# Kernel optimization log

Measured on AMD Instinct MI355X. Metric: run time of the kernel, lower is better.

Reference implementation:

```python
import jax, jax.numpy as jnp
import numpy as np

B, LF, RATE = 2, 2048, 4
DF, DS, H = 1024, 1024, 8
D2 = DF // 2            # 512: both self (d1) and cross (d2) branch dims (equal split)
POOL_H = 2048
TS = LF // RATE         # 512 slow steps


def _p(key, shape):
    return jax.random.normal(key, shape, jnp.float32) * 0.02


def setup_inputs() -> dict:
    keys = iter(jax.random.split(jax.random.key(0), 32))
    inp = {
        "x_fast": jax.random.normal(next(keys), (B, LF, DF), jnp.float32),
        "x_slow": jax.random.normal(next(keys), (B, TS, DS), jnp.float32),
    }
    for name in ("fself", "fcross", "sself", "scross"):
        inp[f"{name}_wqkv"] = _p(next(keys), (D2, 3 * D2))
        inp[f"{name}_bqkv"] = jnp.zeros((3 * D2,), jnp.float32)
        inp[f"{name}_wo"] = _p(next(keys), (D2, D2))
        inp[f"{name}_bo"] = jnp.zeros((D2,), jnp.float32)
    inp["lift_w"] = _p(next(keys), (DS, D2))
    inp["lift_b"] = jnp.zeros((D2,), jnp.float32)
    inp["pool_w1"] = _p(next(keys), (RATE * DF, POOL_H))
    inp["pool_b1"] = jnp.zeros((POOL_H,), jnp.float32)
    inp["pool_w2"] = _p(next(keys), (POOL_H, D2))
    inp["pool_b2"] = jnp.zeros((D2,), jnp.float32)
    return inp


def _mha(q_in, k_in, v_in, wqkv, bqkv, wo, bo):
    """Standard multihead attention with fused in-proj weight [d, 3d]."""
    b, tq, d = q_in.shape
    hd = d // H
    q = q_in @ wqkv[:, :d] + bqkv[:d]
    k = k_in @ wqkv[:, d:2 * d] + bqkv[d:2 * d]
    v = v_in @ wqkv[:, 2 * d:] + bqkv[2 * d:]
    q = q.reshape(b, tq, H, hd)
    k = k.reshape(b, k_in.shape[1], H, hd)
    v = v.reshape(b, v_in.shape[1], H, hd)
    scores = jnp.einsum('bqhd,bkhd->bhqk', q, k) * np.float32(1.0 / np.sqrt(hd))
    w = jax.nn.softmax(scores, axis=-1)
    o = jnp.einsum('bhqk,bkhd->bqhd', w, v).reshape(b, tq, d)
    return o @ wo + bo


def _forward(x_fast, x_slow,
             fself_wqkv, fself_bqkv, fself_wo, fself_bo,
             fcross_wqkv, fcross_bqkv, fcross_wo, fcross_bo,
             sself_wqkv, sself_bqkv, sself_wo, sself_bo,
             scross_wqkv, scross_bqkv, scross_wo, scross_bo,
             lift_w, lift_b, pool_w1, pool_b1, pool_w2, pool_b2):
    b = x_fast.shape[0]
    # ---- fast level: lift slow -> fast timescale (ffn applied before repeat)
    y = jnp.repeat(x_slow @ lift_w + lift_b, RATE, axis=1)          # [B, LF, D2]
    x1, x2 = x_fast[..., :D2], x_fast[..., D2:]
    z_fast = jnp.concatenate([
        _mha(x1, x1, x1, fself_wqkv, fself_bqkv, fself_wo, fself_bo),
        _mha(x2, y, y, fcross_wqkv, fcross_bqkv, fcross_wo, fcross_bo),
    ], axis=-1)
    # ---- slow level: causal block pooling of fast sequence
    blocks = x_fast.reshape(b, TS, RATE * DF)                        # LF == TS*RATE
    s = jax.nn.gelu(blocks @ pool_w1 + pool_b1) @ pool_w2 + pool_b2  # [B, TS, D2]
    # causal shift: prepend zero slow step, drop last (zero in pooled feature dim)
    s = jnp.concatenate([jnp.zeros((b, 1, D2), s.dtype), s[:, :-1]], axis=1)
    s1, s2 = x_slow[..., :D2], x_slow[..., D2:]
    z_slow = jnp.concatenate([
        _mha(s1, s1, s1, sself_wqkv, sself_bqkv, sself_wo, sself_bo),
        _mha(s2, s, s, scross_wqkv, scross_bqkv, scross_wo, scross_bo),
    ], axis=-1)
    return z_fast, z_slow


def reference(x_fast, x_slow,
              fself_wqkv, fself_bqkv, fself_wo, fself_bo,
              fcross_wqkv, fcross_bqkv, fcross_wo, fcross_bo,
              sself_wqkv, sself_bqkv, sself_wo, sself_bo,
              scross_wqkv, scross_bqkv, scross_wo, scross_bo,
              lift_w, lift_b, pool_w1, pool_b1, pool_w2, pool_b2):
    return _forward(x_fast, x_slow,
                    fself_wqkv, fself_bqkv, fself_wo, fself_bo,
                    fcross_wqkv, fcross_bqkv, fcross_wo, fcross_bo,
                    sself_wqkv, sself_bqkv, sself_wo, sself_bo,
                    scross_wqkv, scross_bqkv, scross_wo, scross_bo,
                    lift_w, lift_b, pool_w1, pool_b1, pool_w2, pool_b2)
```

## Files before the change

### kernel.cpp

```cpp
#include <hip/hip_runtime.h>
#include <hip/hip_bf16.h>


typedef __attribute__((ext_vector_type(8))) short bf16x8;
typedef __attribute__((ext_vector_type(4))) float f32x4;
typedef unsigned short u16;
typedef unsigned int u32;

__device__ inline u16 f2bf(float f) {
    __hip_bfloat16 h = __float2bfloat16(f);
    return *reinterpret_cast<u16*>(&h);
}
__device__ inline u32 pack2(float a, float b) {
    return (u32)f2bf(a) | ((u32)f2bf(b) << 16);
}
__device__ inline float bf2f(u16 h) {
    u32 x = ((u32)h) << 16; float f;
    __builtin_memcpy(&f, &x, 4);
    return f;
}
__device__ inline void gld16(const u16* g, u16* l) {
    __builtin_amdgcn_global_load_lds(
        (const __attribute__((address_space(1))) void*)(g),
        (__attribute__((address_space(3))) void*)(l), 16, 0, 0);
}

struct GDesc {
    const u16* A; const u16* Bt; const float* bias;
    void* out0; u16* aux0; u16* aux1;
    int lda, ldb, ldc, K, ntx, mode, rshift, tile_end;
};
struct GPack { int n; int pad[3]; GDesc d[8]; };

template <int TMT>
__global__ __launch_bounds__(256)
void gemm_multi(GPack pk)
{
    constexpr int TM = TMT * 16;
    constexpr int W = TMT / 2;
    __shared__ u16 As[TM * 64];
    __shared__ u16 Bs[TM * 64];

    int bid = blockIdx.x;
    int di = 0;
    while (bid >= pk.d[di].tile_end) ++di;
    const GDesc g = pk.d[di];
    const int base = di ? pk.d[di - 1].tile_end : 0;
    const int local = bid - base;
    const int ty = local / g.ntx, tx = local - ty * g.ntx;
    const int row0 = ty * TM, col0 = tx * TM;

    const int t = threadIdx.x;
    const int wave = t >> 6, lane = t & 63;
    const int l15 = lane & 15, quad = lane >> 4;
    const int wm = (wave >> 1) * W * 16, wn = (wave & 1) * W * 16;

    const int srow = wave * 8 + (lane >> 3);
    const int ssw = (((lane & 7) ^ (lane >> 3))) * 8;
    const u16* Ag = g.A + (long long)(row0 + srow) * g.lda + ssw;
    const u16* Bg = g.Bt + (long long)(col0 + srow) * g.ldb + ssw;

    const int c0 = (quad ^ (l15 & 7)) * 8;

    f32x4 acc[W][W];
#pragma unroll
    for (int i = 0; i < W; ++i)
#pragma unroll
        for (int j = 0; j < W; ++j) {
            acc[i][j][0] = 0.f; acc[i][j][1] = 0.f;
            acc[i][j][2] = 0.f; acc[i][j][3] = 0.f;
        }

    for (int k0 = 0; k0 < g.K; k0 += 64) {
        __syncthreads();
#pragma unroll
        for (int r = 0; r < TM / 32; ++r) {
            gld16(Ag + (long long)r * 32 * g.lda + k0, As + r * 2048 + wave * 512);
            gld16(Bg + (long long)r * 32 * g.ldb + k0, Bs + r * 2048 + wave * 512);
        }
        __syncthreads();
#pragma unroll
        for (int kc = 0; kc < 2; ++kc) {
            const int cc = kc ? (c0 ^ 32) : c0;
            bf16x8 af[W], bfr[W];
#pragma unroll
            for (int i = 0; i < W; ++i) {
                af[i]  = *(const bf16x8*)(As + (wm + i * 16 + l15) * 64 + cc);
                bfr[i] = *(const bf16x8*)(Bs + (wn + i * 16 + l15) * 64 + cc);
            }
#pragma unroll
            for (int i = 0; i < W; ++i)
#pragma unroll
                for (int j = 0; j < W; ++j)
                    acc[i][j] = __builtin_amdgcn_mfma_f32_16x16x32_bf16(af[i], bfr[j], acc[i][j], 0, 0, 0);
        }
    }

    const int rmask = (1 << g.rshift) - 1;
#pragma unroll
    for (int i = 0; i < W; ++i)
#pragma unroll
        for (int j = 0; j < W; ++j)
#pragma unroll
            for (int r = 0; r < 4; ++r) {
                int m = row0 + wm + i * 16 + quad * 4 + r;
                int n = col0 + wn + j * 16 + l15;
                float v = acc[i][j][r];
                if (g.mode != 5) v += g.bias[n];
                if (g.mode == 0) {
                    ((float*)g.out0)[(long long)m * g.ldc + n] = v;
                } else if (g.mode == 1 || g.mode == 5) {
                    ((u16*)g.out0)[(long long)m * g.ldc + n] = f2bf(v);
                } else if (g.mode == 2) {
                    float x3 = v * v * v;
                    v = 0.5f * v * (1.f + tanhf(0.7978845608028654f * (v + 0.044715f * x3)));
                    ((u16*)g.out0)[(long long)m * g.ldc + n] = f2bf(v);
                } else if (g.mode == 3) {
                    u16 h = f2bf(v);
                    if (n < 512) ((u16*)g.out0)[(long long)m * 512 + n] = h;
                    else if (n < 1024) g.aux0[(long long)m * 512 + (n - 512)] = h;
                    else {
                        int d = n - 1024;
                        int bb = m >> g.rshift, rr = m & rmask;
                        g.aux1[((long long)((bb * 8 + (d >> 6)) * 64 + (d & 63)) << g.rshift) + rr] = h;
                    }
                } else if (g.mode == 4) {
                    u16 h = f2bf(v);
                    if (n < 512) ((u16*)g.out0)[(long long)m * 512 + n] = h;
                    else {
                        int d = n - 512;
                        int bb = m >> g.rshift, rr = m & rmask;
                        g.aux1[((long long)((bb * 8 + (d >> 6)) * 64 + (d & 63)) << g.rshift) + rr] = h;
                    }
                } else {
                    int t9 = m & 511;
                    if (t9 != 511) ((u16*)g.out0)[(long long)(m + 1) * g.ldc + n] = f2bf(v);
                    if (t9 == 0)  ((u16*)g.out0)[(long long)m * g.ldc + n] = 0;
                }
            }
}

#define ALD 72

struct ADesc { const u16* Q; const u16* K; const u16* Vt; u16* O; int Rq, nk, tile_end, pad; };
struct APack { int n; int pad[3]; ADesc d[4]; };

__global__ __launch_bounds__(256)
void attn_multi(APack pk, float prescale)
{
    __shared__ u16 Qs[64 * 64];
    __shared__ u16 Ks[64 * 64];
    __shared__ u16 Vts[64 * 64];
    __shared__ u16 Ps[4][16 * ALD];

    int bid = blockIdx.x;
    int di = 0;
    while (bid >= pk.d[di].tile_end) ++di;
    const ADesc g = pk.d[di];
    const int base = di ? pk.d[di - 1].tile_end : 0;
    const int local = bid - base;

    const int t = threadIdx.x;
    const int wave = t >> 6, lane = t & 63;
    const int l15 = lane & 15, quad = lane >> 4;
    const int bh = local & 15, b = bh >> 3, h = bh & 7;
    const int q0 = (local >> 4) * 64;
    const int nk = g.nk;

    const int srow = wave * 8 + (lane >> 3);
    const int ssw = (((lane & 7) ^ (lane >> 3))) * 8;
    const int c0 = (quad ^ (l15 & 7)) * 8;

    const u16* Qg = g.Q + ((long long)(b * g.Rq + q0 + srow) << 9) + h * 64 + ssw;
    const u16* Kg = g.K + ((long long)(b * nk + srow) << 9) + h * 64 + ssw;
    const u16* Vg = g.Vt + (long long)bh * 64 * nk + (long long)srow * nk + ssw;

#pragma unroll
    for (int r = 0; r < 2; ++r)
        gld16(Qg + ((long long)r * 32 << 9), Qs + r * 2048 + wave * 512);
    __syncthreads();

    bf16x8 qf[2];
    qf[0] = *(const bf16x8*)(Qs + (wave * 16 + l15) * 64 + c0);
    qf[1] = *(const bf16x8*)(Qs + (wave * 16 + l15) * 64 + (c0 ^ 32));

    f32x4 Oacc[4];
#pragma unroll
    for (int nt = 0; nt < 4; ++nt) { Oacc[nt][0] = 0.f; Oacc[nt][1] = 0.f; Oacc[nt][2] = 0.f; Oacc[nt][3] = 0.f; }
    float lr[4] = {0.f, 0.f, 0.f, 0.f};

    u16* Pw = &Ps[wave][0];

    for (int kt = 0; kt < nk; kt += 64) {
        __syncthreads();
#pragma unroll
        for (int r = 0; r < 2; ++r) {
            gld16(Kg + ((long long)(kt + r * 32) << 9), Ks + r * 2048 + wave * 512);
            gld16(Vg + (long long)r * 32 * nk + kt, Vts + r * 2048 + wave * 512);
        }
        __syncthreads();

#pragma unroll
        for (int k16 = 0; k16 < 4; ++k16) {
            f32x4 s;
            s[0] = 0.f; s[1] = 0.f; s[2] = 0.f; s[3] = 0.f;
            bf16x8 kf0 = *(const bf16x8*)(Ks + (k16 * 16 + l15) * 64 + c0);
            bf16x8 kf1 = *(const bf16x8*)(Ks + (k16 * 16 + l15) * 64 + (c0 ^ 32));
            s = __builtin_amdgcn_mfma_f32_16x16x32_bf16(qf[0], kf0, s, 0, 0, 0);
            s = __builtin_amdgcn_mfma_f32_16x16x32_bf16(qf[1], kf1, s, 0, 0, 0);
#pragma unroll
            for (int r = 0; r < 4; ++r) {
                float p = exp2f(s[r] * prescale);
                lr[r] += p;
                Pw[(quad * 4 + r) * ALD + k16 * 16 + l15] = f2bf(p);
            }
        }

        bf16x8 pf0 = *(const bf16x8*)(Pw + l15 * ALD + quad * 8);
        bf16x8 pf1 = *(const bf16x8*)(Pw + l15 * ALD + 32 + quad * 8);
#pragma unroll
        for (int nt = 0; nt < 4; ++nt) {
            bf16x8 vf0 = *(const bf16x8*)(Vts + (nt * 16 + l15) * 64 + c0);
            bf16x8 vf1 = *(const bf16x8*)(Vts + (nt * 16 + l15) * 64 + (c0 ^ 32));
            Oacc[nt] = __builtin_amdgcn_mfma_f32_16x16x32_bf16(pf0, vf0, Oacc[nt], 0, 0, 0);
            Oacc[nt] = __builtin_amdgcn_mfma_f32_16x16x32_bf16(pf1, vf1, Oacc[nt], 0, 0, 0);
        }
    }

    float inv[4];
#pragma unroll
    for (int r = 0; r < 4; ++r) {
        float s = lr[r];
#pragma unroll
        for (int off = 1; off < 16; off <<= 1) s += __shfl_xor(s, off);
        inv[r] = 1.f / s;
    }

    u16* Ob = g.O + ((long long)(b * g.Rq + q0 + wave * 16 + quad * 4) << 9) + h * 64;
#pragma unroll
    for (int nt = 0; nt < 4; ++nt)
#pragma unroll
        for (int r = 0; r < 4; ++r)
            Ob[(long long)r * 512 + nt * 16 + l15] = f2bf(Oacc[nt][r] * inv[r]);
}

struct WDesc { const float* src; u16* dst; int ldn, K, tx_, tile_end; };
struct WPack { int n; int pad[3]; WDesc d[12]; };

__global__ __launch_bounds__(256)
void wt_multi(WPack pk)
{
    __shared__ float T[64][68];
    int bid = blockIdx.x;
    int di = 0;
    while (bid >= pk.d[di].tile_end) ++di;
    const WDesc g = pk.d[di];
    const int base = di ? pk.d[di - 1].tile_end : 0;
    const int local = bid - base;
    const int k0 = (local % g.tx_) * 64;
    const int n0 = (local / g.tx_) * 64;
    const int t = threadIdx.x;
#pragma unroll
    for (int i = 0; i < 4; ++i) {
        int idx = t + i * 256;
        int r = idx >> 4, c4 = idx & 15;
        float4 v = *(const float4*)(g.src + (long long)(k0 + r) * g.ldn + n0 + c4 * 4);
        T[r][c4 * 4 + 0] = v.x; T[r][c4 * 4 + 1] = v.y;
        T[r][c4 * 4 + 2] = v.z; T[r][c4 * 4 + 3] = v.w;
    }
    __syncthreads();
#pragma unroll
    for (int i = 0; i < 4; ++i) {
        int idx = t + i * 256;
        int rn = idx >> 4, k4 = idx & 15;
        uint2 u;
        u.x = pack2(T[k4 * 4 + 0][rn], T[k4 * 4 + 1][rn]);
        u.y = pack2(T[k4 * 4 + 2][rn], T[k4 * 4 + 3][rn]);
        *(uint2*)(g.dst + (long long)(n0 + rn) * g.K + k0 + k4 * 4) = u;
    }
}

__global__ __launch_bounds__(256)
void c_cvt2(const float* __restrict__ a, u16* __restrict__ da, int na8,
            const float* __restrict__ b, u16* __restrict__ db)
{
    int i = blockIdx.x * 256 + threadIdx.x;
    const float* s; u16* d;
    if (i < na8) { s = a + (long long)i * 8; d = da + (long long)i * 8; }
    else { s = b + (long long)(i - na8) * 8; d = db + (long long)(i - na8) * 8; }
    float4 x = *(const float4*)s;
    float4 y = *(const float4*)(s + 4);
    uint4 u;
    u.x = pack2(x.x, x.y); u.y = pack2(x.z, x.w);
    u.z = pack2(y.x, y.y); u.w = pack2(y.z, y.w);
    *(uint4*)d = u;
}

__global__ __launch_bounds__(256)
void gelu_sum(u16* __restrict__ p0, const u16* __restrict__ p1,
              const float* __restrict__ bias)
{
    int i8 = (blockIdx.x * 256 + threadIdx.x) * 8;
    uint4 a = *(const uint4*)(p0 + i8);
    uint4 b = *(const uint4*)(p1 + i8);
    int n = i8 & 2047;
    float4 bi0 = *(const float4*)(bias + n);
    float4 bi1 = *(const float4*)(bias + n + 4);
    float bb[8] = {bi0.x, bi0.y, bi0.z, bi0.w, bi1.x, bi1.y, bi1.z, bi1.w};
    u32 aw[4] = {a.x, a.y, a.z, a.w};
    u32 bw[4] = {b.x, b.y, b.z, b.w};
    u32 ow[4];
#pragma unroll
    for (int k = 0; k < 4; ++k) {
        float v0 = bf2f((u16)(aw[k] & 0xffff)) + bf2f((u16)(bw[k] & 0xffff)) + bb[2 * k];
        float v1 = bf2f((u16)(aw[k] >> 16)) + bf2f((u16)(bw[k] >> 16)) + bb[2 * k + 1];
        float x3 = v0 * v0 * v0;
        v0 = 0.5f * v0 * (1.f + tanhf(0.7978845608028654f * (v0 + 0.044715f * x3)));
        x3 = v1 * v1 * v1;
        v1 = 0.5f * v1 * (1.f + tanhf(0.7978845608028654f * (v1 + 0.044715f * x3)));
        ow[k] = pack2(v0, v1);
    }
    uint4 o; o.x = ow[0]; o.y = ow[1]; o.z = ow[2]; o.w = ow[3];
    *(uint4*)(p0 + i8) = o;
}

extern "C" void kernel_launch(void* const* d_in, const int* in_sizes, int n_in,
                              void* d_out, int out_size, void* d_ws, size_t ws_size,
                              hipStream_t stream)
{
    const float* x_fast      = (const float*)d_in[0];
    const float* x_slow      = (const float*)d_in[1];
    const float* fself_wqkv  = (const float*)d_in[2];
    const float* fself_bqkv  = (const float*)d_in[3];
    const float* fself_wo    = (const float*)d_in[4];
    const float* fself_bo    = (const float*)d_in[5];
    const float* fcross_wqkv = (const float*)d_in[6];
    const float* fcross_bqkv = (const float*)d_in[7];
    const float* fcross_wo   = (const float*)d_in[8];
    const float* fcross_bo   = (const float*)d_in[9];
    const float* sself_wqkv  = (const float*)d_in[10];
    const float* sself_bqkv  = (const float*)d_in[11];
    const float* sself_wo    = (const float*)d_in[12];
    const float* sself_bo    = (const float*)d_in[13];
    const float* scross_wqkv = (const float*)d_in[14];
    const float* scross_bqkv = (const float*)d_in[15];
    const float* scross_wo   = (const float*)d_in[16];
    const float* scross_bo   = (const float*)d_in[17];
    const float* lift_w      = (const float*)d_in[18];
    const float* lift_b      = (const float*)d_in[19];
    const float* pool_w1     = (const float*)d_in[20];
    const float* pool_b1     = (const float*)d_in[21];
    const float* pool_w2     = (const float*)d_in[22];
    const float* pool_b2     = (const float*)d_in[23];

    float* out = (float*)d_out;
    float* zf = out;
    float* zs = out + 2LL * 2048 * 1024;

    float* ws = (float*)d_ws;
    u16* pw1T     = (u16*)(ws + 0);
    u16* wqkvT_f  = (u16*)(ws + 4194304);
    u16* wqkvT_c  = (u16*)(ws + 4587520);
    u16* wqkvT_s  = (u16*)(ws + 4980736);
    u16* wqkvT_sc = (u16*)(ws + 5373952);
    u16* liftT    = (u16*)(ws + 5767168);
    u16* pw2T     = (u16*)(ws + 6029312);
    u16* woT_f    = (u16*)(ws + 6553600);
    u16* woT_c    = (u16*)(ws + 6684672);
    u16* woT_s    = (u16*)(ws + 6815744);
    u16* woT_sc   = (u16*)(ws + 6946816);
    u16* xfb      = (u16*)(ws + 7077888);
    u16* xsb      = (u16*)(ws + 9175040);
    u16* q1       = (u16*)(ws + 9699328);
    u16* k1       = (u16*)(ws + 10747904);
    u16* vt1      = (u16*)(ws + 11796480);
    u16* qs       = (u16*)(ws + 12845056);
    u16* ks       = (u16*)(ws + 13107200);
    u16* vts      = (u16*)(ws + 13369344);
    u16* qcs      = (u16*)(ws + 13631488);
    u16* k2    = (u16*)(ws + 0);
    u16* vt2   = (u16*)(ws + 262144);
    u16* sbufS = (u16*)(ws + 524288);
    u16* kcs   = (u16*)(ws + 786432);
    u16* vtcs  = (u16*)(ws + 1048576);
    u16* fo1   = (u16*)(ws + 1310720);
    u16* fo2   = (u16*)(ws + 2359296);
    u16* so1   = (u16*)(ws + 3407872);
    u16* so2   = (u16*)(ws + 3670016);
    u16* q2   = (u16*)(out + 0);
    u16* ybuf = (u16*)(out + 1048576);
    u16* hbuf = (u16*)(out + 1310720);
    u16* p1b  = (u16*)(out + 2359296);

    hipLaunchKernelGGL(c_cvt2, dim3(2560), dim3(256), 0, stream,
                       x_fast, xfb, 524288, x_slow, xsb);

    {
        WPack p; p.n = 11;
        int te = 0, i = 0;
        auto add = [&](const float* s, u16* d, int ldn, int K, int N) {
            te += (K / 64) * (N / 64);
            p.d[i++] = WDesc{s, d, ldn, K, K / 64, te};
        };
        add(pool_w1, pw1T, 2048, 4096, 2048);
        add(fself_wqkv, wqkvT_f, 1536, 512, 1536);
        add(fcross_wqkv, wqkvT_c, 1536, 512, 1536);
        add(sself_wqkv, wqkvT_s, 1536, 512, 1536);
        add(scross_wqkv, wqkvT_sc, 1536, 512, 1536);
        add(lift_w, liftT, 512, 1024, 512);
        add(pool_w2, pw2T, 512, 2048, 512);
        add(fself_wo, woT_f, 512, 512, 512);
        add(fcross_wo, woT_c, 512, 512, 512);
        add(sself_wo, woT_s, 512, 512, 512);
        add(scross_wo, woT_sc, 512, 512, 512);
        hipLaunchKernelGGL(wt_multi, dim3(te), dim3(256), 0, stream, p);
    }

    auto gl = [&](GPack& p, int i, const u16* A, int lda,
                  const u16* Bt, int ldb, const float* bias,
                  void* out0, int ldc, int M, int N, int K, int mode,
                  u16* aux0, u16* aux1, int rshift, int TM, int& te) {
        te += (M / TM) * (N / TM);
        p.d[i] = GDesc{A, Bt, bias, out0, aux0, aux1,
                       lda, ldb, ldc, K, N / TM, mode, rshift, te};
    };

    {
        GPack p; p.n = 7; int te = 0;
        gl(p, 0, xfb, 4096, pw1T, 4096, pool_b1, hbuf, 2048,
           1024, 2048, 2048, 5, 0, 0, 0, 128, te);
        gl(p, 1, xfb + 2048, 4096, pw1T + 2048, 4096, pool_b1, p1b, 2048,
           1024, 2048, 2048, 5, 0, 0, 0, 128, te);
        gl(p, 2, xfb, 1024, wqkvT_f, 512, fself_bqkv, q1, 512,
           4096, 1536, 512, 3, k1, vt1, 11, 128, te);
        gl(p, 3, xfb + 512, 1024, wqkvT_c, 512, fcross_bqkv, q2, 512,
           4096, 512, 512, 1, 0, 0, 0, 128, te);
        gl(p, 4, xsb, 1024, wqkvT_s, 512, sself_bqkv, qs, 512,
           1024, 1536, 512, 3, ks, vts, 9, 128, te);
        gl(p, 5, xsb, 1024, liftT, 1024, lift_b, ybuf, 512,
           1024, 512, 1024, 1, 0, 0, 0, 128, te);
        gl(p, 6, xsb + 512, 1024, wqkvT_sc, 512, scross_bqkv, qcs, 512,
           1024, 512, 512, 1, 0, 0, 0, 128, te);
        hipLaunchKernelGGL(gemm_multi<8>, dim3(te), dim3(256), 0, stream, p);
    }

    hipLaunchKernelGGL(gelu_sum, dim3(1024), dim3(256), 0, stream, hbuf, p1b, pool_b1);

    {
        GPack p; p.n = 2; int te = 0;
        gl(p, 0, ybuf, 512, wqkvT_c + 512 * 512, 512, fcross_bqkv + 512, k2, 512,
           1024, 1024, 512, 4, 0, vt2, 9, 64, te);
        gl(p, 1, hbuf, 2048, pw2T, 2048, pool_b2, sbufS, 512,
           1024, 512, 2048, 6, 0, 0, 0, 64, te);
        hipLaunchKernelGGL(gemm_multi<4>, dim3(te), dim3(256), 0, stream, p);
    }

    {
        GPack p; p.n = 1; int te = 0;
        gl(p, 0, sbufS, 512, wqkvT_sc + 512 * 512, 512, scross_bqkv + 512, kcs, 512,
           1024, 1024, 512, 4, 0, vtcs, 9, 64, te);
        hipLaunchKernelGGL(gemm_multi<4>, dim3(te), dim3(256), 0, stream, p);
    }

    {
        APack p; p.n = 4;
        int te = 0, i = 0;
        auto add = [&](const u16* Q, const u16* K, const u16* Vt, u16* O, int Rq, int nk) {
            te += (Rq / 64) * 16;
            p.d[i++] = ADesc{Q, K, Vt, O, Rq, nk, te, 0};
        };
        add(q1, k1, vt1, fo1, 2048, 2048);
        add(q2, k2, vt2, fo2, 2048, 512);
        add(qs, ks, vts, so1, 512, 512);
        add(qcs, kcs, vtcs, so2, 512, 512);
        hipLaunchKernelGGL(attn_multi, dim3(te), dim3(256), 0, stream, p,
                           0.125f * 1.4426950408889634f);
    }

    {
        GPack p; p.n = 4; int te = 0;
        gl(p, 0, fo1, 512, woT_f, 512, fself_bo, zf, 1024,
           4096, 512, 512, 0, 0, 0, 0, 128, te);
        gl(p, 1, fo2, 512, woT_c, 512, fcross_bo, zf + 512, 1024,
           4096, 512, 512, 0, 0, 0, 0, 128, te);
        gl(p, 2, so1, 512, woT_s, 512, sself_bo, zs, 1024,
           1024, 512, 512, 0, 0, 0, 0, 128, te);
        gl(p, 3, so2, 512, woT_sc, 512, scross_bo, zs + 512, 1024,
           1024, 512, 512, 0, 0, 0, 0, 128, te);
        hipLaunchKernelGGL(gemm_multi<8>, dim3(te), dim3(256), 0, stream, p);
    }
}
```

Measured before the change: 358.3 us.

## Double-buffer LDS tiles in GEMM and attention kernels to overlap loads with MFMA

Both the multi-GEMM kernel and the attention kernel now keep two LDS buffers for their operand tiles. The next K-tile is issued with global_load_lds while the MFMAs run on the current buffer, which cuts the barriers per tile from two to one. In attention, the Q tile is staged into the second K buffer to save LDS. The loops assume K and nk are multiples of 128, and the doubled LDS footprint may reduce occupancy.

```diff
diff --git a/kernel.cpp b/kernel.cpp
--- a/kernel.cpp
+++ b/kernel.cpp
@@ -38,8 +38,9 @@
 {
     constexpr int TM = TMT * 16;
     constexpr int W = TMT / 2;
-    __shared__ u16 As[TM * 64];
-    __shared__ u16 Bs[TM * 64];
+    constexpr int BUF = TM * 64;
+    __shared__ u16 As[2 * BUF];
+    __shared__ u16 Bs[2 * BUF];
 
     int bid = blockIdx.x;
     int di = 0;
@@ -71,22 +72,24 @@
             acc[i][j][2] = 0.f; acc[i][j][3] = 0.f;
         }
 
-    for (int k0 = 0; k0 < g.K; k0 += 64) {
-        __syncthreads();
+    auto stage = [&](int buf, int k0) {
 #pragma unroll
         for (int r = 0; r < TM / 32; ++r) {
-            gld16(Ag + (long long)r * 32 * g.lda + k0, As + r * 2048 + wave * 512);
-            gld16(Bg + (long long)r * 32 * g.ldb + k0, Bs + r * 2048 + wave * 512);
+            gld16(Ag + (long long)r * 32 * g.lda + k0, As + buf * BUF + r * 2048 + wave * 512);
+            gld16(Bg + (long long)r * 32 * g.ldb + k0, Bs + buf * BUF + r * 2048 + wave * 512);
         }
-        __syncthreads();
+    };
+    auto compute = [&](int buf) {
+        const u16* Ab = As + buf * BUF;
+        const u16* Bb = Bs + buf * BUF;
 #pragma unroll
         for (int kc = 0; kc < 2; ++kc) {
             const int cc = kc ? (c0 ^ 32) : c0;
             bf16x8 af[W], bfr[W];
 #pragma unroll
             for (int i = 0; i < W; ++i) {
-                af[i]  = *(const bf16x8*)(As + (wm + i * 16 + l15) * 64 + cc);
-                bfr[i] = *(const bf16x8*)(Bs + (wn + i * 16 + l15) * 64 + cc);
+                af[i]  = *(const bf16x8*)(Ab + (wm + i * 16 + l15) * 64 + cc);
+                bfr[i] = *(const bf16x8*)(Bb + (wn + i * 16 + l15) * 64 + cc);
             }
 #pragma unroll
             for (int i = 0; i < W; ++i)
@@ -94,7 +97,19 @@
                 for (int j = 0; j < W; ++j)
                     acc[i][j] = __builtin_amdgcn_mfma_f32_16x16x32_bf16(af[i], bfr[j], acc[i][j], 0, 0, 0);
         }
-    }
+    };
+
+    stage(0, 0);
+    __syncthreads();
+    const int npairs = g.K >> 7;
+    int k0 = 64;
+    for (int s = 0; s < npairs - 1; ++s) {
+        stage(1, k0);       compute(0); __syncthreads();
+        stage(0, k0 + 64);  compute(1); __syncthreads();
+        k0 += 128;
+    }
+    stage(1, k0); compute(0); __syncthreads();
+    compute(1);
 
     const int rmask = (1 << g.rshift) - 1;
 #pragma unroll
@@ -148,9 +163,8 @@
 __global__ __launch_bounds__(256)
 void attn_multi(APack pk, float prescale)
 {
-    __shared__ u16 Qs[64 * 64];
-    __shared__ u16 Ks[64 * 64];
-    __shared__ u16 Vts[64 * 64];
+    __shared__ u16 Ks[2 * 64 * 64];
+    __shared__ u16 Vts[2 * 64 * 64];
     __shared__ u16 Ps[4][16 * ALD];
 
     int bid = blockIdx.x;
@@ -177,12 +191,12 @@
 
 #pragma unroll
     for (int r = 0; r < 2; ++r)
-        gld16(Qg + ((long long)r * 32 << 9), Qs + r * 2048 + wave * 512);
+        gld16(Qg + ((long long)r * 32 << 9), Ks + 4096 + r * 2048 + wave * 512);
     __syncthreads();
 
     bf16x8 qf[2];
-    qf[0] = *(const bf16x8*)(Qs + (wave * 16 + l15) * 64 + c0);
-    qf[1] = *(const bf16x8*)(Qs + (wave * 16 + l15) * 64 + (c0 ^ 32));
+    qf[0] = *(const bf16x8*)(Ks + 4096 + (wave * 16 + l15) * 64 + c0);
+    qf[1] = *(const bf16x8*)(Ks + 4096 + (wave * 16 + l15) * 64 + (c0 ^ 32));
 
     f32x4 Oacc[4];
 #pragma unroll
@@ -191,21 +205,22 @@
 
     u16* Pw = &Ps[wave][0];
 
-    for (int kt = 0; kt < nk; kt += 64) {
-        __syncthreads();
+    auto stage = [&](int buf, int kt) {
 #pragma unroll
         for (int r = 0; r < 2; ++r) {
-            gld16(Kg + ((long long)(kt + r * 32) << 9), Ks + r * 2048 + wave * 512);
-            gld16(Vg + (long long)r * 32 * nk + kt, Vts + r * 2048 + wave * 512);
+            gld16(Kg + ((long long)(kt + r * 32) << 9), Ks + buf * 4096 + r * 2048 + wave * 512);
+            gld16(Vg + (long long)r * 32 * nk + kt, Vts + buf * 4096 + r * 2048 + wave * 512);
         }
-        __syncthreads();
-
+    };
+    auto acompute = [&](int buf) {
+        const u16* Kb = Ks + buf * 4096;
+        const u16* Vb = Vts + buf * 4096;
 #pragma unroll
         for (int k16 = 0; k16 < 4; ++k16) {
             f32x4 s;
             s[0] = 0.f; s[1] = 0.f; s[2] = 0.f; s[3] = 0.f;
-            bf16x8 kf0 = *(const bf16x8*)(Ks + (k16 * 16 + l15) * 64 + c0);
-            bf16x8 kf1 = *(const bf16x8*)(Ks + (k16 * 16 + l15) * 64 + (c0 ^ 32));
+            bf16x8 kf0 = *(const bf16x8*)(Kb + (k16 * 16 + l15) * 64 + c0);
+            bf16x8 kf1 = *(const bf16x8*)(Kb + (k16 * 16 + l15) * 64 + (c0 ^ 32));
             s = __builtin_amdgcn_mfma_f32_16x16x32_bf16(qf[0], kf0, s, 0, 0, 0);
             s = __builtin_amdgcn_mfma_f32_16x16x32_bf16(qf[1], kf1, s, 0, 0, 0);
 #pragma unroll
@@ -215,17 +230,28 @@
                 Pw[(quad * 4 + r) * ALD + k16 * 16 + l15] = f2bf(p);
             }
         }
-
         bf16x8 pf0 = *(const bf16x8*)(Pw + l15 * ALD + quad * 8);
         bf16x8 pf1 = *(const bf16x8*)(Pw + l15 * ALD + 32 + quad * 8);
 #pragma unroll
         for (int nt = 0; nt < 4; ++nt) {
-            bf16x8 vf0 = *(const bf16x8*)(Vts + (nt * 16 + l15) * 64 + c0);
-            bf16x8 vf1 = *(const bf16x8*)(Vts + (nt * 16 + l15) * 64 + (c0 ^ 32));
+            bf16x8 vf0 = *(const bf16x8*)(Vb + (nt * 16 + l15) * 64 + c0);
+            bf16x8 vf1 = *(const bf16x8*)(Vb + (nt * 16 + l15) * 64 + (c0 ^ 32));
             Oacc[nt] = __builtin_amdgcn_mfma_f32_16x16x32_bf16(pf0, vf0, Oacc[nt], 0, 0, 0);
             Oacc[nt] = __builtin_amdgcn_mfma_f32_16x16x32_bf16(pf1, vf1, Oacc[nt], 0, 0, 0);
         }
-    }
+    };
+
+    stage(0, 0);
+    __syncthreads();
+    const int npairs = nk >> 7;
+    int kt = 64;
+    for (int s2 = 0; s2 < npairs - 1; ++s2) {
+        stage(1, kt);       acompute(0); __syncthreads();
+        stage(0, kt + 64);  acompute(1); __syncthreads();
+        kt += 128;
+    }
+    stage(1, kt); acompute(0); __syncthreads();
+    acompute(1);
 
     float inv[4];
 #pragma unroll
```

New measurement: 364.3 us. Within noise of the previous version (+1.7%).
